# Optimization experiments

Hardware: AMD Instinct MI355X
Metric: run time of the kernel (lower is better)

The kernel has to match this reference:

```python
import jax, jax.numpy as jnp
import numpy as np

NUM_CLASSES = 80
NUM_ANCHORS = 9
NUM_CONVS = 4
FOCAL_ALPHA = 0.25
FOCAL_GAMMA = 2.0
LOSS_NORMALIZER = 100.0
LOSS_WEIGHT = 1.0
LEVEL_SHAPES = [(128, 128), (64, 64), (32, 32), (16, 16), (8, 8)]
C = 256
B = 2
N_TOTAL = NUM_ANCHORS * sum(h * w for h, w in LEVEL_SHAPES)  # 196416


def setup_inputs() -> dict:
    key = jax.random.key(0)
    ks = iter(jax.random.split(key, 32))
    inp = {}
    for i, (h, w) in enumerate(LEVEL_SHAPES):
        inp[f"feat{i}"] = jax.random.normal(next(ks), (B, h, w, C), dtype=jnp.float32)
    inp["anchor_labels"] = jax.random.randint(next(ks), (B, N_TOTAL), -1, NUM_CLASSES + 1, dtype=jnp.int32)
    inp["anchor_deltas"] = jax.random.normal(next(ks), (B, N_TOTAL, 4), dtype=jnp.float32)
    s = 0.05
    inp["in_proj_w"] = s * jax.random.normal(next(ks), (5, C, C), dtype=jnp.float32)  # [lvl, in, out]
    inp["in_proj_b"] = s * jax.random.normal(next(ks), (5, C), dtype=jnp.float32)
    inp["cls_convs_w"] = s * jax.random.normal(next(ks), (NUM_CONVS, 3, 3, C, C), dtype=jnp.float32)  # HWIO
    inp["cls_convs_b"] = s * jax.random.normal(next(ks), (NUM_CONVS, C), dtype=jnp.float32)
    inp["cls_score_w"] = s * jax.random.normal(next(ks), (3, 3, C, NUM_ANCHORS * NUM_CLASSES), dtype=jnp.float32)
    inp["cls_score_b"] = s * jax.random.normal(next(ks), (NUM_ANCHORS * NUM_CLASSES,), dtype=jnp.float32)
    inp["box_convs_w"] = s * jax.random.normal(next(ks), (NUM_CONVS, 3, 3, C, C), dtype=jnp.float32)
    inp["box_convs_b"] = s * jax.random.normal(next(ks), (NUM_CONVS, C), dtype=jnp.float32)
    inp["box_pred_w"] = s * jax.random.normal(next(ks), (3, 3, C, NUM_ANCHORS * 4), dtype=jnp.float32)
    inp["box_pred_b"] = s * jax.random.normal(next(ks), (NUM_ANCHORS * 4,), dtype=jnp.float32)
    return inp


def _conv(x, w, b):
    # x: [B,H,W,Cin] NHWC, w: [3,3,Cin,Cout] HWIO, stride 1, SAME padding
    y = jax.lax.conv_general_dilated(x, w, (1, 1), "SAME",
                                     dimension_numbers=("NHWC", "HWIO", "NHWC"))
    return y + b


def _head(feats, in_proj_w, in_proj_b, cls_convs_w, cls_convs_b, cls_score_w,
          cls_score_b, box_convs_w, box_convs_b, box_pred_w, box_pred_b):
    logit_maps, delta_maps = [], []
    for i, feat in enumerate(feats):  # fixed 5 FPN levels
        x = feat @ in_proj_w[i] + in_proj_b[i]  # in_proj Linear
        c = x
        for j in range(NUM_CONVS):
            c = jax.nn.relu(_conv(c, cls_convs_w[j], cls_convs_b[j]))
        logit = _conv(c, cls_score_w, cls_score_b)  # [B,H,W,A*K]
        d = x
        for j in range(NUM_CONVS):
            d = jax.nn.relu(_conv(d, box_convs_w[j], box_convs_b[j]))
        delta = _conv(d, box_pred_w, box_pred_b)  # [B,H,W,A*4]
        b, h, w, _ = logit.shape
        # reshape_pred_map: [B,H,W,A,P] -> [B, H*W*A, P] (channel c = a*P + p matches NHWC)
        logit_maps.append(logit.reshape(b, h * w * NUM_ANCHORS, NUM_CLASSES))
        delta_maps.append(delta.reshape(b, h * w * NUM_ANCHORS, 4))
    return jnp.concatenate(logit_maps, axis=1), jnp.concatenate(delta_maps, axis=1)


def reference(feat0, feat1, feat2, feat3, feat4, anchor_labels, anchor_deltas,
              in_proj_w, in_proj_b, cls_convs_w, cls_convs_b, cls_score_w,
              cls_score_b, box_convs_w, box_convs_b, box_pred_w, box_pred_b):
    logits, deltas = _head([feat0, feat1, feat2, feat3, feat4], in_proj_w,
                           in_proj_b, cls_convs_w, cls_convs_b, cls_score_w,
                           cls_score_b, box_convs_w, box_convs_b, box_pred_w,
                           box_pred_b)
    # classification: focal loss over anchors with label >= 0 (ignore label -1)
    class_mask = anchor_labels >= 0  # [B,N]
    safe_labels = jnp.where(class_mask, anchor_labels, NUM_CLASSES)
    targets = jax.nn.one_hot(safe_labels, NUM_CLASSES + 1, dtype=logits.dtype)[..., :NUM_CLASSES]
    # stable BCE-with-logits
    ce = jnp.maximum(logits, 0) - logits * targets + jnp.log1p(jnp.exp(-jnp.abs(logits)))
    p = jax.nn.sigmoid(logits)
    p_t = p * targets + (1 - p) * (1 - targets)
    loss = ce * (1 - p_t) ** FOCAL_GAMMA
    alpha_t = FOCAL_ALPHA * targets + (1 - FOCAL_ALPHA) * (1 - targets)
    loss = alpha_t * loss
    cls_loss = jnp.sum(loss * class_mask[..., None]) * (LOSS_WEIGHT / LOSS_NORMALIZER)
    box_mask = class_mask & (anchor_labels != NUM_CLASSES)
    l1 = jnp.abs(deltas - anchor_deltas)
    box_loss = jnp.sum(l1 * box_mask[..., None]) * (LOSS_WEIGHT / LOSS_NORMALIZER)
    return jnp.stack([cls_loss, box_loss])  # [ret_cls_loss, ret_box_loss]
```

## Files before the change

### kernel.cpp

```cpp
#include <hip/hip_runtime.h>
#include <hip/hip_bf16.h>

using bf16 = __hip_bfloat16;
typedef short short8 __attribute__((ext_vector_type(8)));
typedef short short4v __attribute__((ext_vector_type(4)));
typedef float f32x16 __attribute__((ext_vector_type(16)));

#define NT 196416

__device__ __forceinline__ void gload16(const bf16* g, char* l) {
  __builtin_amdgcn_global_load_lds((const __attribute__((address_space(1))) void*)g,
                                   (__attribute__((address_space(3))) void*)l, 16, 0, 0);
}

template <int N> __device__ __forceinline__ void vmw() {
  asm volatile("s_waitcnt vmcnt(%0)" ::"n"(N) : "memory");
}

__global__ void prep_w(const float* __restrict__ src, bf16* __restrict__ dst,
                       int Cout, int NB, int TAPS, int layers, long sstride) {
  const long spl = (long)NB * 16 * 2 * TAPS * 128;
  const long total = spl * layers;
  for (long s = blockIdx.x * (long)blockDim.x + threadIdx.x; s < total;
       s += (long)gridDim.x * blockDim.x) {
    long layer = s / spl;
    long r = s - layer * spl;
    int col = (int)(r & 127);
    long q = r >> 7;
    int t = (int)(q % TAPS); q /= TAPS;
    int c = (int)(q & 1); q >>= 1;
    int k = (int)(q & 15);
    int nb = (int)(q >> 4);
    int co = nb * 128 + col;
    short8 v = {};
    if (co < Cout) {
      const float* p = src + layer * sstride + ((long)(t * 256 + k * 16 + c * 8)) * Cout + co;
#pragma unroll
      for (int j = 0; j < 8; ++j) {
        union { bf16 b; short s16; } u;
        u.b = __float2bfloat16(p[(long)j * Cout]);
        v[j] = u.s16;
      }
    }
    *(short8*)(dst + s * 8) = v;
  }
}

__global__ void halo_kernel(bf16* __restrict__ base, long BS, int W, int nbuf) {
  const int P = 2 * (W + 2) + 2 * W;
  const long n = (long)nbuf * 2 * P * 256;
  for (long t = blockIdx.x * (long)blockDim.x + threadIdx.x; t < n;
       t += (long)gridDim.x * blockDim.x) {
    int ch = (int)(t & 255);
    long q = t >> 8;
    int pix = (int)(q % P);
    int q2 = (int)(q / P);
    int img = q2 & 1;
    int buf = q2 >> 1;
    int row, col;
    if (pix < W + 2) { row = 0; col = pix; }
    else if (pix < 2 * (W + 2)) { row = W + 1; col = pix - (W + 2); }
    else { int e = pix - 2 * (W + 2); row = 1 + (e >> 1); col = (e & 1) ? W + 1 : 0; }
    bf16* p = base + buf * BS + ((long)(img * (W + 2) + row) * (W + 2) + col) * 256 + ch;
    union { bf16 b; short s16; } u; u.s16 = 0;
    *p = u.b;
  }
}

__global__ void cast_feat_kernel(const float* __restrict__ in, bf16* __restrict__ out,
                                 int wshift) {
  const int W = 1 << wshift;
  const long n4 = 2L * W * W * 64;
  for (long t = blockIdx.x * (long)blockDim.x + threadIdx.x; t < n4;
       t += (long)gridDim.x * blockDim.x) {
    int c4 = (int)(t & 63);
    long q = t >> 6;
    int w = (int)(q & (W - 1));
    long q2 = q >> wshift;
    int h = (int)(q2 & (W - 1));
    int b = (int)(q2 >> wshift);
    const float4 f = *(const float4*)(in + (((long)(b * W + h) * W + w) * 256 + c4 * 4));
    short4v v;
    union { bf16 b16; short s16; } u;
    u.b16 = __float2bfloat16(f.x); v[0] = u.s16;
    u.b16 = __float2bfloat16(f.y); v[1] = u.s16;
    u.b16 = __float2bfloat16(f.z); v[2] = u.s16;
    u.b16 = __float2bfloat16(f.w); v[3] = u.s16;
    *(short4v*)(out + (((long)(b * (W + 2) + h + 1) * (W + 2) + w + 1) * 256 + c4 * 4)) = v;
  }
}


#define MFMA_(a, b, c) __builtin_amdgcn_mfma_f32_32x32x16_bf16((a), (b), (c), 0, 0, 0)

#define STAGE_M(cc, ldsb)                                                        \
  do {                                                                           \
    _Pragma("unroll") for (int i_ = 0; i_ < UPW; ++i_) {                         \
      const int u_ = wid + NW * i_;                                              \
      if (u_ < UA) {                                                             \
        const int cg_ = (u_ >= PG) ? 1 : 0;                                      \
        const int pu_ = (u_ - cg_ * PG) * 64;                                    \
        gload16(gA + ((long)(pu_ + lane) * 256 + cg_ * 8 + (cc) * 16),           \
                (ldsb) + (cg_ * PPA + pu_) * 16);                                \
      } else {                                                                   \
        const int s0_ = (u_ - UA) * 64;                                          \
        gload16(gB + (long)(cc) * (TAPS * 2048) + (s0_ + lane) * 8,              \
                (ldsb) + ABYTES + s0_ * 16);                                     \
      }                                                                          \
    }                                                                            \
  } while (0)

#define COMPUTE_M(ldsb)                                                          \
  do {                                                                           \
    _Pragma("unroll") for (int t_ = 0; t_ < TAPS; ++t_) {                        \
      const int TOFF_ = (TAPS == 9) ? ((((t_) / 3) * (W + 2) + ((t_) % 3)) * 16) \
                                    : ((W + 3) * 16);                            \
      const short8 b0_ = *(const short8*)((ldsb) + b16_0 + (t_) * 2048);         \
      const short8 b1_ = *(const short8*)((ldsb) + b16_1 + (t_) * 2048);         \
      {                                                                          \
        const short8 a_ = *(const short8*)((ldsb) + a16_0 + TOFF_);              \
        c0a = MFMA_(a_, b0_, c0a); c0b = MFMA_(a_, b1_, c0b);                    \
      }                                                                          \
      {                                                                          \
        const short8 a_ = *(const short8*)((ldsb) + a16_1 + TOFF_);              \
        c1a = MFMA_(a_, b0_, c1a); c1b = MFMA_(a_, b1_, c1b);                    \
      }                                                                          \
      if constexpr (MFR > 2) {                                                   \
        {                                                                        \
          const short8 a_ = *(const short8*)((ldsb) + a16_2 + TOFF_);            \
          c2a = MFMA_(a_, b0_, c2a); c2b = MFMA_(a_, b1_, c2b);                  \
        }                                                                        \
        {                                                                        \
          const short8 a_ = *(const short8*)((ldsb) + a16_3 + TOFF_);            \
          c3a = MFMA_(a_, b0_, c3a); c3b = MFMA_(a_, b1_, c3b);                  \
        }                                                                        \
      }                                                                          \
    }                                                                            \
  } while (0)

#define AOFF_(mf_)                                                               \
  ((lh * PPA + (((wm * (MFR * 32) + (mf_) * 32 + l31) >> WSH) * (W + 2)) +       \
    ((wm * (MFR * 32) + (mf_) * 32 + l31) & (W - 1))) * 16)

#define STORE_PAIR(mf_, accv, nf_)                                               \
  do {                                                                           \
    const int co_ = n0 + wn * 64 + (nf_) * 32 + l31;                             \
    const float bv_ = bias[co_];                                                 \
    _Pragma("unroll") for (int r_ = 0; r_ < 16; ++r_) {                          \
      const int mrow_ =                                                          \
          wm * (MFR * 32) + (mf_) * 32 + (r_ & 3) + 8 * (r_ >> 2) + 4 * lh;      \
      const int rr_ = rb * BM + mrow_;                                           \
      const int h_ = rr_ >> WSH;                                                 \
      const int w_ = rr_ & (W - 1);                                              \
      float v_ = accv[r_] + bv_;                                                 \
      if (TAPS == 9) v_ = fmaxf(v_, 0.f);                                        \
      outp[((long)(img * (W + 2) + h_ + 1) * (W + 2) + (w_ + 1)) * 256 + co_] =  \
          __float2bfloat16(v_);                                                  \
    }                                                                            \
  } while (0)

#define LOSS_PAIR(mf_, accv, nf_)                                                \
  do {                                                                           \
    const int co_ = n0 + wn * 64 + (nf_) * 32 + l31;                             \
    if (co_ < Cout) {                                                            \
      const float bv_ = bias[co_];                                               \
      int aidx_, sub_;                                                           \
      if constexpr (EPI == 1) { aidx_ = co_ / 80; sub_ = co_ - aidx_ * 80; }     \
      else { aidx_ = co_ >> 2; sub_ = co_ & 3; }                                 \
      _Pragma("unroll") for (int r_ = 0; r_ < 16; ++r_) {                        \
        const int mrow_ =                                                        \
            wm * (MFR * 32) + (mf_) * 32 + (r_ & 3) + 8 * (r_ >> 2) + 4 * lh;    \
        const int label_ = lsh[mrow_ * 9 + aidx_];                               \
        const float z_ = accv[r_] + bv_;                                         \
        if constexpr (EPI == 1) {                                                \
          if (label_ >= 0) {                                                     \
            const float tt_ = (label_ == sub_) ? 1.f : 0.f;                      \
            const float ce_ = fmaxf(z_, 0.f) - z_ * tt_ + log1pf(expf(-fabsf(z_))); \
            const float p_ = 1.f / (1.f + expf(-z_));                            \
            const float pt_ = p_ * tt_ + (1.f - p_) * (1.f - tt_);               \
            const float om_ = 1.f - pt_;                                         \
            lsum += (0.25f * tt_ + 0.75f * (1.f - tt_)) * ce_ * om_ * om_;       \
          }                                                                      \
        } else {                                                                 \
          if (label_ >= 0 && label_ != 80) {                                     \
            lsum += fabsf(z_ - dsh[(mrow_ * 9 + aidx_) * 4 + sub_]);             \
          }                                                                      \
        }                                                                        \
      }                                                                          \
    }                                                                            \
  } while (0)

template <int WSH, int WM, int WN, int MFR, int TAPS, int EPI, int DBUF>
__global__ __launch_bounds__(WM * WN * 64) void conv_t(
    const bf16* __restrict__ inA, const bf16* __restrict__ inB,
    const bf16* __restrict__ wpA, const bf16* __restrict__ wpB,
    const float* __restrict__ biasA, const float* __restrict__ biasB,
    bf16* __restrict__ outA, bf16* __restrict__ outB,
    const int* __restrict__ labels, const float* __restrict__ tdel,
    int abase, float* __restrict__ lout, int Cout, int nbHalf) {
  constexpr int W = 1 << WSH;
  constexpr int NW = WM * WN;
  constexpr int BM = WM * MFR * 32;
  constexpr int R = BM >> WSH;
  constexpr int PP = (R + 2) * (W + 2);
  constexpr int PPA0 = ((PP + 63) / 64) * 64;
  constexpr int PPA = (NW == 4 && (PPA0 % 128)) ? PPA0 + 64 : PPA0;
  constexpr int PG = PPA / 64;
  constexpr int UA = PPA / 32;
  constexpr int UB = TAPS * 4;
  constexpr int U = UA + UB;
  static_assert(U % NW == 0, "unit padding");
  constexpr int UPW = U / NW;
  constexpr int ABYTES = 2 * PPA * 16;
  constexpr int BUFB = ABYTES + TAPS * 4096;

  __shared__ __align__(16) char smem[BUFB * (DBUF ? 2 : 1)];

  const int tid = threadIdx.x;
  const int lane = tid & 63;
  const int wid = tid >> 6;
  const int wm = wid / WN;
  const int wn = wid % WN;
  const int l31 = lane & 31;
  const int lh = lane >> 5;

  const int yb = blockIdx.y;
  const int half = (yb >= nbHalf) ? 1 : 0;
  const int nb = yb - half * nbHalf;
  const int n0 = nb * 128;
  const int rb = blockIdx.x;
  const int img = blockIdx.z;

  const bf16* in = half ? inB : inA;
  const bf16* wp = half ? wpB : wpA;
  const float* bias = half ? biasB : biasA;
  bf16* outp = half ? outB : outA;

  const bf16* gA = in + (long)(img * (W + 2) + rb * R) * ((W + 2) * 256);
  const bf16* gB = wp + (long)nb * (TAPS * 32768);

  const int a16_0 = AOFF_(0);
  const int a16_1 = AOFF_(1);
  const int a16_2 = (MFR > 2) ? AOFF_(2) : 0;
  const int a16_3 = (MFR > 2) ? AOFF_(3) : 0;
  const int b16_0 = ABYTES + (lh * (TAPS * 128) + wn * 64 + l31) * 16;
  const int b16_1 = ABYTES + (lh * (TAPS * 128) + wn * 64 + 32 + l31) * 16;

  f32x16 c0a = (f32x16)(0.f), c0b = (f32x16)(0.f);
  f32x16 c1a = (f32x16)(0.f), c1b = (f32x16)(0.f);
  f32x16 c2a = (f32x16)(0.f), c2b = (f32x16)(0.f);
  f32x16 c3a = (f32x16)(0.f), c3b = (f32x16)(0.f);

  if constexpr (DBUF) {
    char* bb0 = smem;
    char* bb1 = smem + BUFB;
    STAGE_M(0, bb0);
#pragma unroll 1
    for (int i = 0; i < 8; ++i) {
      STAGE_M(2 * i + 1, bb1);
      vmw<UPW>();
      __builtin_amdgcn_s_barrier();
      COMPUTE_M(bb0);
      __builtin_amdgcn_s_barrier();
      if (i < 7) {
        STAGE_M(2 * i + 2, bb0);
        vmw<UPW>();
      } else {
        vmw<0>();
      }
      __builtin_amdgcn_s_barrier();
      COMPUTE_M(bb1);
      __builtin_amdgcn_s_barrier();
    }
  } else {
#pragma unroll 1
    for (int cc = 0; cc < 16; ++cc) {
      __syncthreads();
      STAGE_M(cc, smem);
      __syncthreads();
      COMPUTE_M(smem);
    }
  }

  if constexpr (EPI == 0) {
    STORE_PAIR(0, c0a, 0); STORE_PAIR(0, c0b, 1);
    STORE_PAIR(1, c1a, 0); STORE_PAIR(1, c1b, 1);
    if constexpr (MFR > 2) {
      STORE_PAIR(2, c2a, 0); STORE_PAIR(2, c2b, 1);
      STORE_PAIR(3, c3a, 0); STORE_PAIR(3, c3b, 1);
    }
  } else {
    __syncthreads();
    int* lsh = (int*)smem;
    float* dsh = (float*)(smem + BM * 9 * 4);
    const long lbase = (long)img * NT + abase + (long)rb * BM * 9;
    for (int i = tid; i < BM * 9; i += NW * 64) lsh[i] = labels[lbase + i];
    if constexpr (EPI == 2) {
      for (int i = tid; i < BM * 9 * 4; i += NW * 64) dsh[i] = tdel[lbase * 4 + i];
    }
    __syncthreads();

    float lsum = 0.f;
    LOSS_PAIR(0, c0a, 0); LOSS_PAIR(0, c0b, 1);
    LOSS_PAIR(1, c1a, 0); LOSS_PAIR(1, c1b, 1);
    if constexpr (MFR > 2) {
      LOSS_PAIR(2, c2a, 0); LOSS_PAIR(2, c2b, 1);
      LOSS_PAIR(3, c3a, 0); LOSS_PAIR(3, c3b, 1);
    }
#pragma unroll
    for (int off = 32; off > 0; off >>= 1) lsum += __shfl_down(lsum, off, 64);
    __syncthreads();
    float* red = (float*)smem;
    if (lane == 0) red[wid] = lsum;
    __syncthreads();
    if (tid == 0) {
      float s = 0.f;
      for (int i = 0; i < NW; ++i) s += red[i];
      atomicAdd(lout, s * 0.01f);
    }
  }
}

static inline int igrid(long n, int cap) {
  long g = (n + 255) / 256;
  return (int)(g > cap ? cap : g);
}

struct LvlArgs {
  bf16* bufs; long BS;
  const bf16 *wip, *wcls, *wbox, *wsc, *wpred;
  const float *ipb, *ccb, *csb, *bcb, *bpb;
  const int* labels; const float* tdel;
  int abase; float* out;
};

template <int WSH, int WM, int WN, int MFR, int TDB>
static void run_level(const LvlArgs& A, bool merged, hipStream_t s) {
  constexpr int W = 1 << WSH;
  constexpr int BM = WM * MFR * 32;
  const int m = (W * W) / BM;
  dim3 blk(WM * WN * 64);
  if (merged) {
    bf16* xb = A.bufs;
    bf16* c0 = A.bufs + A.BS;
    bf16* c1 = A.bufs + 2 * A.BS;
    bf16* d0 = A.bufs + 3 * A.BS;
    bf16* d1 = A.bufs + 4 * A.BS;
    conv_t<WSH, WM, WN, MFR, 1, 0, 1><<<dim3(m, 2, 2), blk, 0, s>>>(
        c1, c1, A.wip, A.wip, A.ipb, A.ipb, xb, xb, nullptr, nullptr, 0, nullptr, 256, 2);
    const bf16* ci = xb; const bf16* bi = xb;
    bf16* co_[4] = {c0, c1, c0, c1};
    bf16* bo_[4] = {d0, d1, d0, d1};
    for (int j = 0; j < 4; ++j) {
      conv_t<WSH, WM, WN, MFR, 9, 0, TDB><<<dim3(m, 4, 2), blk, 0, s>>>(
          ci, bi, A.wcls + (long)j * 589824, A.wbox + (long)j * 589824,
          A.ccb + j * 256, A.bcb + j * 256, co_[j], bo_[j],
          nullptr, nullptr, 0, nullptr, 256, 2);
      ci = co_[j]; bi = bo_[j];
    }
    conv_t<WSH, WM, WN, MFR, 9, 1, TDB><<<dim3(m, 6, 2), blk, 0, s>>>(
        ci, ci, A.wsc, A.wsc, A.csb, A.csb, nullptr, nullptr,
        A.labels, nullptr, A.abase, A.out + 0, 720, 6);
    conv_t<WSH, WM, WN, MFR, 9, 2, TDB><<<dim3(m, 1, 2), blk, 0, s>>>(
        bi, bi, A.wpred, A.wpred, A.bpb, A.bpb, nullptr, nullptr,
        A.labels, A.tdel, A.abase, A.out + 1, 36, 1);
  } else {
    bf16* xb = A.bufs;
    bf16* t0 = A.bufs + A.BS;
    bf16* t1 = A.bufs + 2 * A.BS;
    conv_t<WSH, WM, WN, MFR, 1, 0, 1><<<dim3(m, 2, 2), blk, 0, s>>>(
        t0, t0, A.wip, A.wip, A.ipb, A.ipb, xb, xb, nullptr, nullptr, 0, nullptr, 256, 2);
    for (int br = 0; br < 2; ++br) {
      const bf16* wt = br ? A.wbox : A.wcls;
      const float* bb = br ? A.bcb : A.ccb;
      const bf16* ci = xb;
      bf16* oo[4] = {t1, t0, t1, t0};
      for (int j = 0; j < 4; ++j) {
        conv_t<WSH, WM, WN, MFR, 9, 0, TDB><<<dim3(m, 2, 2), blk, 0, s>>>(
            ci, ci, wt + (long)j * 589824, wt + (long)j * 589824, bb + j * 256, bb + j * 256,
            oo[j], oo[j], nullptr, nullptr, 0, nullptr, 256, 2);
        ci = oo[j];
      }
      if (br == 0)
        conv_t<WSH, WM, WN, MFR, 9, 1, TDB><<<dim3(m, 6, 2), blk, 0, s>>>(
            t0, t0, A.wsc, A.wsc, A.csb, A.csb, nullptr, nullptr,
            A.labels, nullptr, A.abase, A.out + 0, 720, 6);
      else
        conv_t<WSH, WM, WN, MFR, 9, 2, TDB><<<dim3(m, 1, 2), blk, 0, s>>>(
            t0, t0, A.wpred, A.wpred, A.bpb, A.bpb, nullptr, nullptr,
            A.labels, A.tdel, A.abase, A.out + 1, 36, 1);
    }
  }
}

extern "C" void kernel_launch(void* const* d_in, const int* in_sizes, int n_in,
                              void* d_out, int out_size, void* d_ws, size_t ws_size,
                              hipStream_t stream) {
  const float* feat_in[5] = {(const float*)d_in[0], (const float*)d_in[1],
                             (const float*)d_in[2], (const float*)d_in[3],
                             (const float*)d_in[4]};
  const int* labels = (const int*)d_in[5];
  const float* adeltas = (const float*)d_in[6];
  const float* ipw = (const float*)d_in[7];
  const float* ipb = (const float*)d_in[8];
  const float* ccw = (const float*)d_in[9];
  const float* ccb = (const float*)d_in[10];
  const float* csw = (const float*)d_in[11];
  const float* csb = (const float*)d_in[12];
  const float* bcw = (const float*)d_in[13];
  const float* bcb = (const float*)d_in[14];
  const float* bpw = (const float*)d_in[15];
  const float* bpb = (const float*)d_in[16];
  float* out = (float*)d_out;

  const long BUFE = 2L * 130 * 130 * 256;
  const long GAP = 65536;
  const long BS = BUFE + GAP;
  const long WELEMS = 327680 + 2359296 + 2359296 + 1769472 + 294912;
  const bool merged = ws_size >= (size_t)((5 * BS + WELEMS) * 2);
  const int nbuf = merged ? 5 : 3;

  bf16* ws = (bf16*)d_ws;
  bf16* wp_ip = ws + nbuf * BS;
  bf16* wp_cls = wp_ip + 327680;
  bf16* wp_box = wp_cls + 2359296;
  bf16* wp_sc = wp_box + 2359296;
  bf16* wp_pred = wp_sc + 1769472;

  hipMemsetAsync(d_out, 0, 2 * sizeof(float), stream);

  prep_w<<<igrid(5L * 8192, 1024), 256, 0, stream>>>(ipw, wp_ip, 256, 2, 1, 5, 65536);
  prep_w<<<igrid(4L * 73728, 1024), 256, 0, stream>>>(ccw, wp_cls, 256, 2, 9, 4, 589824);
  prep_w<<<igrid(4L * 73728, 1024), 256, 0, stream>>>(bcw, wp_box, 256, 2, 9, 4, 589824);
  prep_w<<<igrid(221184L, 1024), 256, 0, stream>>>(csw, wp_sc, 720, 6, 9, 1, 0);
  prep_w<<<igrid(36864L, 1024), 256, 0, stream>>>(bpw, wp_pred, 36, 1, 9, 1, 0);

  static const int LS[5] = {7, 6, 5, 4, 3};
  static const int AB[5] = {0, 147456, 184320, 193536, 195840};

  bf16* featsBuf = ws + (merged ? 2 : 1) * BS;

  for (int l = 0; l < 5; ++l) {
    const int W = 1 << LS[l];
    halo_kernel<<<igrid((long)nbuf * 2 * (4 * W + 4) * 256, 2048), 256, 0, stream>>>(
        ws, BS, W, nbuf);
    cast_feat_kernel<<<igrid(2L * W * W * 64, 2048), 256, 0, stream>>>(
        feat_in[l], featsBuf, LS[l]);

    LvlArgs A;
    A.bufs = ws; A.BS = BS;
    A.wip = wp_ip + (long)l * 65536; A.ipb = ipb + l * 256;
    A.wcls = wp_cls; A.wbox = wp_box; A.wsc = wp_sc; A.wpred = wp_pred;
    A.ccb = ccb; A.csb = csb; A.bcb = bcb; A.bpb = bpb;
    A.labels = labels; A.tdel = adeltas; A.abase = AB[l]; A.out = out;

    switch (l) {
      case 0: run_level<7, 2, 2, 4, 0>(A, merged, stream); break;
      case 1: run_level<6, 2, 2, 2, 1>(A, merged, stream); break;
      case 2: run_level<5, 1, 2, 2, 1>(A, merged, stream); break;
      case 3: run_level<4, 1, 2, 2, 1>(A, merged, stream); break;
      case 4: run_level<3, 1, 2, 2, 1>(A, merged, stream); break;
    }
  }
}
```

Before: 1.808 ms.

## Switch activations to channel-planar bf16 layout and always double-buffer conv tiles

Activation buffers move from NHWC (256 channels contiguous per pixel) to 32 planes of 8 channels each, so every 16-byte staging load for a channel chunk reads a contiguous run of pixels instead of striding by 512 bytes. The halo, cast and store epilogues are updated to the new addressing. The single-buffer path is removed, so every conv now double-buffers in LDS, and the level-0 tile uses 4 warps in M instead of 2. LDS padding is computed by a helper so the number of load units divides evenly across warps. The per-element bf16 output stores in the epilogue now stride by 8 elements across planes, which may cost store efficiency, and the larger LDS footprint at level 0 may reduce occupancy.

```diff
diff --git a/kernel.cpp b/kernel.cpp
--- a/kernel.cpp
+++ b/kernel.cpp
@@ -15,6 +15,12 @@
 
 template <int N> __device__ __forceinline__ void vmw() {
   asm volatile("s_waitcnt vmcnt(%0)" ::"n"(N) : "memory");
+}
+
+constexpr int pick_ppa(int PP, int UB, int NW) {
+  int p = ((PP + 63) / 64) * 64;
+  while (((p / 32 + UB) % NW) != 0) p += 64;
+  return p;
 }
 
 __global__ void prep_w(const float* __restrict__ src, bf16* __restrict__ dst,
@@ -48,6 +54,7 @@
 
 __global__ void halo_kernel(bf16* __restrict__ base, long BS, int W, int nbuf) {
   const int P = 2 * (W + 2) + 2 * W;
+  const long PLSZ8 = (long)(W + 2) * (W + 2) * 8;
   const long n = (long)nbuf * 2 * P * 256;
   for (long t = blockIdx.x * (long)blockDim.x + threadIdx.x; t < n;
        t += (long)gridDim.x * blockDim.x) {
@@ -61,7 +68,8 @@
     if (pix < W + 2) { row = 0; col = pix; }
     else if (pix < 2 * (W + 2)) { row = W + 1; col = pix - (W + 2); }
     else { int e = pix - 2 * (W + 2); row = 1 + (e >> 1); col = (e & 1) ? W + 1 : 0; }
-    bf16* p = base + buf * BS + ((long)(img * (W + 2) + row) * (W + 2) + col) * 256 + ch;
+    bf16* p = base + buf * BS + ((long)(img * 32 + (ch >> 3))) * PLSZ8 +
+              ((long)row * (W + 2) + col) * 8 + (ch & 7);
     union { bf16 b; short s16; } u; u.s16 = 0;
     *p = u.b;
   }
@@ -70,6 +78,7 @@
 __global__ void cast_feat_kernel(const float* __restrict__ in, bf16* __restrict__ out,
                                  int wshift) {
   const int W = 1 << wshift;
+  const long PLSZ8 = (long)(W + 2) * (W + 2) * 8;
   const long n4 = 2L * W * W * 64;
   for (long t = blockIdx.x * (long)blockDim.x + threadIdx.x; t < n4;
        t += (long)gridDim.x * blockDim.x) {
@@ -86,7 +95,8 @@
     u.b16 = __float2bfloat16(f.y); v[1] = u.s16;
     u.b16 = __float2bfloat16(f.z); v[2] = u.s16;
     u.b16 = __float2bfloat16(f.w); v[3] = u.s16;
-    *(short4v*)(out + (((long)(b * (W + 2) + h + 1) * (W + 2) + w + 1) * 256 + c4 * 4)) = v;
+    *(short4v*)(out + ((long)(b * 32 + (c4 >> 1))) * PLSZ8 +
+                ((long)(h + 1) * (W + 2) + (w + 1)) * 8 + (c4 & 1) * 4) = v;
   }
 }
 
@@ -98,9 +108,9 @@
     _Pragma("unroll") for (int i_ = 0; i_ < UPW; ++i_) {                         \
       const int u_ = wid + NW * i_;                                              \
       if (u_ < UA) {                                                             \
-        const int cg_ = (u_ >= PG) ? 1 : 0;                                      \
-        const int pu_ = (u_ - cg_ * PG) * 64;                                    \
-        gload16(gA + ((long)(pu_ + lane) * 256 + cg_ * 8 + (cc) * 16),           \
+        const int cg_ = (u_ >= UAH) ? 1 : 0;                                     \
+        const int pu_ = (u_ - cg_ * UAH) * 64;                                   \
+        gload16(gA + (long)((cc) * 2 + cg_) * PLSZ8 + (pu_ + lane) * 8,          \
                 (ldsb) + (cg_ * PPA + pu_) * 16);                                \
       } else {                                                                   \
         const int s0_ = (u_ - UA) * 64;                                          \
@@ -146,6 +156,7 @@
   do {                                                                           \
     const int co_ = n0 + wn * 64 + (nf_) * 32 + l31;                             \
     const float bv_ = bias[co_];                                                 \
+    const long pl_ = ((long)(img * 32 + (co_ >> 3))) * PLSZ8 + (co_ & 7);        \
     _Pragma("unroll") for (int r_ = 0; r_ < 16; ++r_) {                          \
       const int mrow_ =                                                          \
           wm * (MFR * 32) + (mf_) * 32 + (r_ & 3) + 8 * (r_ >> 2) + 4 * lh;      \
@@ -154,7 +165,7 @@
       const int w_ = rr_ & (W - 1);                                              \
       float v_ = accv[r_] + bv_;                                                 \
       if (TAPS == 9) v_ = fmaxf(v_, 0.f);                                        \
-      outp[((long)(img * (W + 2) + h_ + 1) * (W + 2) + (w_ + 1)) * 256 + co_] =  \
+      outp[pl_ + ((long)(h_ + 1) * (W + 2) + (w_ + 1)) * 8] =                    \
           __float2bfloat16(v_);                                                  \
     }                                                                            \
   } while (0)
@@ -190,7 +201,7 @@
     }                                                                            \
   } while (0)
 
-template <int WSH, int WM, int WN, int MFR, int TAPS, int EPI, int DBUF>
+template <int WSH, int WM, int WN, int MFR, int TAPS, int EPI>
 __global__ __launch_bounds__(WM * WN * 64) void conv_t(
     const bf16* __restrict__ inA, const bf16* __restrict__ inB,
     const bf16* __restrict__ wpA, const bf16* __restrict__ wpB,
@@ -203,18 +214,16 @@
   constexpr int BM = WM * MFR * 32;
   constexpr int R = BM >> WSH;
   constexpr int PP = (R + 2) * (W + 2);
-  constexpr int PPA0 = ((PP + 63) / 64) * 64;
-  constexpr int PPA = (NW == 4 && (PPA0 % 128)) ? PPA0 + 64 : PPA0;
-  constexpr int PG = PPA / 64;
+  constexpr long PLSZ8 = (long)(W + 2) * (W + 2) * 8;
+  constexpr int PPA = pick_ppa(PP, TAPS * 4, NW);
+  constexpr int UAH = PPA / 64;
   constexpr int UA = PPA / 32;
-  constexpr int UB = TAPS * 4;
-  constexpr int U = UA + UB;
-  static_assert(U % NW == 0, "unit padding");
+  constexpr int U = UA + TAPS * 4;
   constexpr int UPW = U / NW;
-  constexpr int ABYTES = 2 * PPA * 16;
+  constexpr int ABYTES = PPA * 32;
   constexpr int BUFB = ABYTES + TAPS * 4096;
 
-  __shared__ __align__(16) char smem[BUFB * (DBUF ? 2 : 1)];
+  __shared__ __align__(16) char smem[BUFB * 2];
 
   const int tid = threadIdx.x;
   const int lane = tid & 63;
@@ -236,7 +245,7 @@
   const float* bias = half ? biasB : biasA;
   bf16* outp = half ? outB : outA;
 
-  const bf16* gA = in + (long)(img * (W + 2) + rb * R) * ((W + 2) * 256);
+  const bf16* gA = in + (long)img * 32 * PLSZ8 + (long)(rb * R) * (W + 2) * 8;
   const bf16* gB = wp + (long)nb * (TAPS * 32768);
 
   const int a16_0 = AOFF_(0);
@@ -251,7 +260,7 @@
   f32x16 c2a = (f32x16)(0.f), c2b = (f32x16)(0.f);
   f32x16 c3a = (f32x16)(0.f), c3b = (f32x16)(0.f);
 
-  if constexpr (DBUF) {
+  {
     char* bb0 = smem;
     char* bb1 = smem + BUFB;
     STAGE_M(0, bb0);
@@ -272,14 +281,6 @@
       COMPUTE_M(bb1);
       __builtin_amdgcn_s_barrier();
     }
-  } else {
-#pragma unroll 1
-    for (int cc = 0; cc < 16; ++cc) {
-      __syncthreads();
-      STAGE_M(cc, smem);
-      __syncthreads();
-      COMPUTE_M(smem);
-    }
   }
 
   if constexpr (EPI == 0) {
@@ -334,7 +335,7 @@
   int abase; float* out;
 };
 
-template <int WSH, int WM, int WN, int MFR, int TDB>
+template <int WSH, int WM, int WN, int MFR>
 static void run_level(const LvlArgs& A, bool merged, hipStream_t s) {
   constexpr int W = 1 << WSH;
   constexpr int BM = WM * MFR * 32;
@@ -346,29 +347,29 @@
     bf16* c1 = A.bufs + 2 * A.BS;
     bf16* d0 = A.bufs + 3 * A.BS;
     bf16* d1 = A.bufs + 4 * A.BS;
-    conv_t<WSH, WM, WN, MFR, 1, 0, 1><<<dim3(m, 2, 2), blk, 0, s>>>(
+    conv_t<WSH, WM, WN, MFR, 1, 0><<<dim3(m, 2, 2), blk, 0, s>>>(
         c1, c1, A.wip, A.wip, A.ipb, A.ipb, xb, xb, nullptr, nullptr, 0, nullptr, 256, 2);
     const bf16* ci = xb; const bf16* bi = xb;
     bf16* co_[4] = {c0, c1, c0, c1};
     bf16* bo_[4] = {d0, d1, d0, d1};
     for (int j = 0; j < 4; ++j) {
-      conv_t<WSH, WM, WN, MFR, 9, 0, TDB><<<dim3(m, 4, 2), blk, 0, s>>>(
+      conv_t<WSH, WM, WN, MFR, 9, 0><<<dim3(m, 4, 2), blk, 0, s>>>(
           ci, bi, A.wcls + (long)j * 589824, A.wbox + (long)j * 589824,
           A.ccb + j * 256, A.bcb + j * 256, co_[j], bo_[j],
           nullptr, nullptr, 0, nullptr, 256, 2);
       ci = co_[j]; bi = bo_[j];
     }
-    conv_t<WSH, WM, WN, MFR, 9, 1, TDB><<<dim3(m, 6, 2), blk, 0, s>>>(
+    conv_t<WSH, WM, WN, MFR, 9, 1><<<dim3(m, 6, 2), blk, 0, s>>>(
         ci, ci, A.wsc, A.wsc, A.csb, A.csb, nullptr, nullptr,
         A.labels, nullptr, A.abase, A.out + 0, 720, 6);
-    conv_t<WSH, WM, WN, MFR, 9, 2, TDB><<<dim3(m, 1, 2), blk, 0, s>>>(
+    conv_t<WSH, WM, WN, MFR, 9, 2><<<dim3(m, 1, 2), blk, 0, s>>>(
         bi, bi, A.wpred, A.wpred, A.bpb, A.bpb, nullptr, nullptr,
         A.labels, A.tdel, A.abase, A.out + 1, 36, 1);
   } else {
     bf16* xb = A.bufs;
     bf16* t0 = A.bufs + A.BS;
     bf16* t1 = A.bufs + 2 * A.BS;
-    conv_t<WSH, WM, WN, MFR, 1, 0, 1><<<dim3(m, 2, 2), blk, 0, s>>>(
+    conv_t<WSH, WM, WN, MFR, 1, 0><<<dim3(m, 2, 2), blk, 0, s>>>(
         t0, t0, A.wip, A.wip, A.ipb, A.ipb, xb, xb, nullptr, nullptr, 0, nullptr, 256, 2);
     for (int br = 0; br < 2; ++br) {
       const bf16* wt = br ? A.wbox : A.wcls;
@@ -376,17 +377,17 @@
       const bf16* ci = xb;
       bf16* oo[4] = {t1, t0, t1, t0};
       for (int j = 0; j < 4; ++j) {
-        conv_t<WSH, WM, WN, MFR, 9, 0, TDB><<<dim3(m, 2, 2), blk, 0, s>>>(
+        conv_t<WSH, WM, WN, MFR, 9, 0><<<dim3(m, 2, 2), blk, 0, s>>>(
             ci, ci, wt + (long)j * 589824, wt + (long)j * 589824, bb + j * 256, bb + j * 256,
             oo[j], oo[j], nullptr, nullptr, 0, nullptr, 256, 2);
         ci = oo[j];
       }
       if (br == 0)
-        conv_t<WSH, WM, WN, MFR, 9, 1, TDB><<<dim3(m, 6, 2), blk, 0, s>>>(
+        conv_t<WSH, WM, WN, MFR, 9, 1><<<dim3(m, 6, 2), blk, 0, s>>>(
             t0, t0, A.wsc, A.wsc, A.csb, A.csb, nullptr, nullptr,
             A.labels, nullptr, A.abase, A.out + 0, 720, 6);
       else
-        conv_t<WSH, WM, WN, MFR, 9, 2, TDB><<<dim3(m, 1, 2), blk, 0, s>>>(
+        conv_t<WSH, WM, WN, MFR, 9, 2><<<dim3(m, 1, 2), blk, 0, s>>>(
             t0, t0, A.wpred, A.wpred, A.bpb, A.bpb, nullptr, nullptr,
             A.labels, A.tdel, A.abase, A.out + 1, 36, 1);
     }
@@ -455,11 +456,11 @@
     A.labels = labels; A.tdel = adeltas; A.abase = AB[l]; A.out = out;
 
     switch (l) {
-      case 0: run_level<7, 2, 2, 4, 0>(A, merged, stream); break;
-      case 1: run_level<6, 2, 2, 2, 1>(A, merged, stream); break;
-      case 2: run_level<5, 1, 2, 2, 1>(A, merged, stream); break;
-      case 3: run_level<4, 1, 2, 2, 1>(A, merged, stream); break;
-      case 4: run_level<3, 1, 2, 2, 1>(A, merged, stream); break;
-    }
-  }
-}
+      case 0: run_level<7, 4, 2, 4>(A, merged, stream); break;
+      case 1: run_level<6, 2, 2, 2>(A, merged, stream); break;
+      case 2: run_level<5, 1, 2, 2>(A, merged, stream); break;
+      case 3: run_level<4, 1, 2, 2>(A, merged, stream); break;
+      case 4: run_level<3, 1, 2, 2>(A, merged, stream); break;
+    }
+  }
+}
```

After: 1.520 ms. 1.19x faster.
